# Performance work log

Measured on AMD Instinct MI355X. Metric: run time of the kernel, lower is better.

## Reference

```python
import jax, jax.numpy as jnp
import numpy as np

ROPE_THETA = 10000.0


def _rotate_half(x):
    # interleaved rotation: out[..., 2i] = -x[..., 2i+1], out[..., 2i+1] = x[..., 2i]
    x_even = x[..., ::2]
    x_odd = x[..., 1::2]
    return jnp.stack([-x_odd, x_even], axis=-1).reshape(x.shape)


def _rope_cos_sin(N, D, dtype):
    inv_freq = 1.0 / (ROPE_THETA ** (jnp.arange(0, D, 2, dtype=jnp.float32) / D))  # [D/2]
    angles = jnp.arange(N, dtype=jnp.float32)[:, None] * inv_freq[None, :]          # [N, D/2]
    angles = jnp.repeat(angles, 2, axis=-1)                                          # [N, D]
    cos = jnp.cos(angles).astype(dtype)[None, :, None, :]  # [1, N, 1, D]
    sin = jnp.sin(angles).astype(dtype)[None, :, None, :]
    return cos, sin


def setup_inputs() -> dict:
    key = jax.random.key(0)
    kq, kk, kv, km = jax.random.split(key, 4)
    B, N, H, D = 16, 1024, 8, 64
    xq = jax.random.normal(kq, (B, N, H, D), dtype=jnp.float32)
    xk = jax.random.normal(kk, (B, N, H, D), dtype=jnp.float32)
    xv = jax.random.normal(kv, (B, N, H, D), dtype=jnp.float32)
    vis_mask = jax.random.bernoulli(km, 0.8, (B, N))  # bool visibility mask per batch
    return {"xq": xq, "xk": xk, "xv": xv, "vis_mask": vis_mask}


def reference(xq, xk, xv, vis_mask):
    B, N, H, D = xq.shape
    sm_scale = 1.0 / np.sqrt(D).astype(np.float32)

    # RoPE (interleaved) on q and k
    cos, sin = _rope_cos_sin(N, D, xq.dtype)
    q = xq * cos + _rotate_half(xq) * sin
    k = xk * cos + _rotate_half(xk) * sin

    # masked full attention: scores [B, H, N, N]
    scores = jnp.einsum("bnhd,bmhd->bhnm", q, k) * sm_scale
    attn_mask = (vis_mask[:, None, :, None] & vis_mask[:, None, None, :])  # [B,1,N,N]
    scores = jnp.where(attn_mask, scores, -jnp.inf)
    p = jax.nn.softmax(scores, axis=-1)
    p = jnp.nan_to_num(p, nan=0.0)  # fully-masked rows -> zeros (matches fallback)
    out = jnp.einsum("bhnm,bmhd->bnhd", p, xv)
    return out
```

## Files before the change

kernel.cpp:

```cpp
#include <hip/hip_runtime.h>
#include <hip/hip_bf16.h>
#include <stdint.h>

#define Bb 16
#define Nn 1024
#define Hh 8
#define Dd 64

typedef unsigned short u16;
typedef float f32x4 __attribute__((ext_vector_type(4)));
typedef short short8 __attribute__((ext_vector_type(8)));

union U4S8 { uint4 u; short8 s; };
union BF2U { __hip_bfloat162 h; uint32_t u; };

__device__ __forceinline__ uint32_t f2bf(float f){
  union{float f;uint32_t i;} v; v.f=f;
  return (v.i + 0x7fffu + ((v.i>>16)&1u))>>16;
}

__device__ __forceinline__ f32x4 mfma16(short8 a, short8 b, f32x4 c){
  return __builtin_amdgcn_mfma_f32_16x16x32_bf16(a,b,c,0,0,0);
}

#define ROPE_K 0.41524101186092030f
#define QS 0.18033688011112042f
#define NEGBIG -1.0e30f

__global__ void rope_table_kernel(float2* __restrict__ tab){
  int id = blockIdx.x*256 + threadIdx.x;
  int n = id >> 5, i = id & 31;
  float inv = exp2f(-(float)i * ROPE_K);
  float a = (float)n * inv;
  float s, c; sincosf(a, &s, &c);
  tab[id] = make_float2(c, s);
}

__global__ __launch_bounds__(256) void prepass_kernel(
    const float* __restrict__ xk, const float* __restrict__ xv,
    const float2* __restrict__ tab,
    u16* __restrict__ Kr, u16* __restrict__ Vp)
{
  const int tid = threadIdx.x;
  const int bid = blockIdx.x;
  const int nt = bid & 15, h = (bid>>4)&7, b = bid>>7;
  const size_t bh = (size_t)b*Hh + h;

  {
    int r = tid>>2, c = (tid&3)<<4;
    int n = (nt<<6) + r;
    const float4* g = (const float4*)(xk + ((((size_t)b*Nn + n)*Hh + h)<<6) + c);
    float4 a0=g[0],a1=g[1],a2=g[2],a3=g[3];
    float xx[16] = {a0.x,a0.y,a0.z,a0.w, a1.x,a1.y,a1.z,a1.w,
                    a2.x,a2.y,a2.z,a2.w, a3.x,a3.y,a3.z,a3.w};
    uint32_t w[8];
    #pragma unroll
    for (int j=0;j<8;++j){
      int i = (c>>1)+j;
      float cs, sn;
      if (tab){ float2 t = tab[(n<<5)+i]; cs = t.x; sn = t.y; }
      else { float inv = exp2f(-(float)i * ROPE_K); sincosf((float)n*inv, &sn, &cs); }
      float x0 = xx[2*j], x1 = xx[2*j+1];
      float q0 = x0*cs - x1*sn;
      float q1 = x1*cs + x0*sn;
      w[j] = f2bf(q0) | (f2bf(q1)<<16);
    }
    u16* dst = Kr + (((bh<<10) + (size_t)n)<<6) + c;
    *(uint4*)dst     = make_uint4(w[0],w[1],w[2],w[3]);
    *(uint4*)(dst+8) = make_uint4(w[4],w[5],w[6],w[7]);
  }

  {
    int k = tid&63, ds = (tid>>6)<<4;
    int n = (nt<<6) + k;
    int slot = (k&1) | (((k>>4)&3)<<1) | (((k>>2)&3)<<3) | (((k>>1)&1)<<5);
    const float4* g = (const float4*)(xv + ((((size_t)b*Nn + n)*Hh + h)<<6) + ds);
    float4 a0=g[0],a1=g[1],a2=g[2],a3=g[3];
    float vv[16] = {a0.x,a0.y,a0.z,a0.w, a1.x,a1.y,a1.z,a1.w,
                    a2.x,a2.y,a2.z,a2.w, a3.x,a3.y,a3.z,a3.w};
    #pragma unroll
    for (int j=0;j<16;++j)
      Vp[ (bh<<16) + (nt<<12) + ((size_t)(ds+j)<<6) + slot ] = (u16)f2bf(vv[j]);
  }
}

__global__ __launch_bounds__(256,4) void attn4_kernel(
    const float* __restrict__ xq, const u16* __restrict__ Kr,
    const u16* __restrict__ Vp, const int* __restrict__ vis,
    const float2* __restrict__ tab, float* __restrict__ out)
{
  __shared__ u16 Ks[64][72];
  __shared__ u16 Vs[64][72];

  const int tid  = threadIdx.x;
  const int wave = tid >> 6;
  const int lane = tid & 63;
  const int l15  = lane & 15;
  const int quad = lane >> 4;

  const int bid = blockIdx.x;
  const int qt = bid & 7;
  const int h  = (bid >> 3) & 7;
  const int b  = bid >> 6;
  const size_t bh = (size_t)b*Hh + h;
  const int qbase = qt<<7;

  const int* visb = vis + b*Nn;

  short8 qa[2][2];
  #pragma unroll
  for (int mb=0; mb<2; ++mb){
    int n = qbase + (wave<<5) + (mb<<4) + l15;
    const float* src = xq + ((((size_t)b*Nn + n)*Hh + h)<<6);
    #pragma unroll
    for (int half=0; half<2; ++half){
      int d0 = (half<<5) + (quad<<3);
      const float4* g = (const float4*)(src + d0);
      float4 u0 = g[0], u1 = g[1];
      float xx[8] = {u0.x,u0.y,u0.z,u0.w, u1.x,u1.y,u1.z,u1.w};
      uint32_t w[4];
      #pragma unroll
      for (int j=0;j<4;++j){
        int i = (d0>>1) + j;
        float cs, sn;
        if (tab){ float2 t = tab[(n<<5)+i]; cs = t.x; sn = t.y; }
        else { float inv = exp2f(-(float)i * ROPE_K); sincosf((float)n*inv, &sn, &cs); }
        float x0 = xx[2*j], x1 = xx[2*j+1];
        float q0 = (x0*cs - x1*sn)*QS;
        float q1 = (x1*cs + x0*sn)*QS;
        w[j] = f2bf(q0) | (f2bf(q1)<<16);
      }
      U4S8 t; t.u = make_uint4(w[0],w[1],w[2],w[3]);
      qa[mb][half] = t.s;
    }
  }

  U4S8 ones_u; ones_u.u = make_uint4(0x3F803F80u,0x3F803F80u,0x3F803F80u,0x3F803F80u);
  const short8 ones = ones_u.s;

  f32x4 acc[2][4];
  f32x4 l_acc[2];
  #pragma unroll
  for (int mb=0;mb<2;++mb){
    l_acc[mb] = (f32x4){0.f,0.f,0.f,0.f};
    #pragma unroll
    for (int s=0;s<4;++s) acc[mb][s] = (f32x4){0.f,0.f,0.f,0.f};
  }

  const u16* Krb = Kr + (bh<<16);
  const u16* Vpb = Vp + (bh<<16);
  const int r = tid>>2, c16 = (tid&3)<<4;

  for (int kt=0; kt<16; ++kt){
    __syncthreads();
    {
      const u16* ksrc = Krb + (kt<<12) + (r<<6) + c16;
      uint4 k0 = *(const uint4*)ksrc, k1 = *(const uint4*)(ksrc+8);
      const u16* vsrc = Vpb + (kt<<12) + (r<<6) + c16;
      uint4 v0 = *(const uint4*)vsrc, v1 = *(const uint4*)(vsrc+8);
      *(uint4*)&Ks[r][c16]   = k0; *(uint4*)&Ks[r][c16+8] = k1;
      *(uint4*)&Vs[r][c16]   = v0; *(uint4*)&Vs[r][c16+8] = v1;
    }
    __syncthreads();

    uint32_t pk[4][2][2];
    #pragma unroll
    for (int kb=0;kb<4;++kb){
      short8 kf0 = *(const short8*)&Ks[(kb<<4)+l15][quad<<3];
      short8 kf1 = *(const short8*)&Ks[(kb<<4)+l15][(quad<<3)+32];
      int4 vi = *(const int4*)&visb[(kt<<6)+(kb<<4)+(quad<<2)];
      f32x4 bias;
      bias.x = vi.x ? 0.f : NEGBIG;
      bias.y = vi.y ? 0.f : NEGBIG;
      bias.z = vi.z ? 0.f : NEGBIG;
      bias.w = vi.w ? 0.f : NEGBIG;
      #pragma unroll
      for (int mb=0;mb<2;++mb){
        f32x4 t = mfma16(kf0, qa[mb][0], bias);
        t = mfma16(kf1, qa[mb][1], t);
        float p0 = __builtin_amdgcn_exp2f(t.x);
        float p1 = __builtin_amdgcn_exp2f(t.y);
        float p2 = __builtin_amdgcn_exp2f(t.z);
        float p3 = __builtin_amdgcn_exp2f(t.w);
        BF2U e0; e0.h = __float22bfloat162_rn(make_float2(p0,p1));
        BF2U e1; e1.h = __float22bfloat162_rn(make_float2(p2,p3));
        pk[kb][0][mb] = e0.u;
        pk[kb][1][mb] = e1.u;
      }
    }

    short8 pa[2][2];
    #pragma unroll
    for (int mb=0;mb<2;++mb){
      U4S8 a0; a0.u = make_uint4(pk[0][0][mb], pk[1][0][mb], pk[2][0][mb], pk[3][0][mb]);
      U4S8 a1; a1.u = make_uint4(pk[0][1][mb], pk[1][1][mb], pk[2][1][mb], pk[3][1][mb]);
      pa[mb][0] = a0.s; pa[mb][1] = a1.s;
    }

    #pragma unroll
    for (int mb=0;mb<2;++mb){
      l_acc[mb] = mfma16(pa[mb][0], ones, l_acc[mb]);
      l_acc[mb] = mfma16(pa[mb][1], ones, l_acc[mb]);
    }
    #pragma unroll
    for (int s=0;s<4;++s){
      short8 vb0 = *(const short8*)&Vs[(s<<4)+l15][quad<<3];
      short8 vb1 = *(const short8*)&Vs[(s<<4)+l15][(quad<<3)+32];
      #pragma unroll
      for (int mb=0;mb<2;++mb){
        acc[mb][s] = mfma16(pa[mb][0], vb0, acc[mb][s]);
        acc[mb][s] = mfma16(pa[mb][1], vb1, acc[mb][s]);
      }
    }
  }

  #pragma unroll
  for (int mb=0;mb<2;++mb){
    int4 qvi = *(const int4*)&visb[qbase + (wave<<5) + (mb<<4) + (quad<<2)];
    int qv[4] = {qvi.x, qvi.y, qvi.z, qvi.w};
    #pragma unroll
    for (int rr=0;rr<4;++rr){
      float lq = l_acc[mb][rr];
      float invl = (qv[rr] != 0 && lq > 0.f) ? 1.f/lq : 0.f;
      int qrow = qbase + (wave<<5) + (mb<<4) + (quad<<2) + rr;
      float* ob = out + ((((size_t)b*Nn + qrow)*Hh + h)<<6);
      #pragma unroll
      for (int s=0;s<4;++s)
        ob[(s<<4)+l15] = acc[mb][s][rr]*invl;
    }
  }
}

__device__ __forceinline__ void stage_rope_row_fb(const float* __restrict__ src,
                                                  u16 (*dst)[72],
                                                  int n_global, int sr, int d0)
{
  const float4* g = (const float4*)src;
  float4 a0 = g[0], a1 = g[1], a2 = g[2], a3 = g[3];
  float xx[16] = {a0.x,a0.y,a0.z,a0.w, a1.x,a1.y,a1.z,a1.w,
                  a2.x,a2.y,a2.z,a2.w, a3.x,a3.y,a3.z,a3.w};
  uint32_t w[8];
  #pragma unroll
  for (int j=0;j<8;++j){
    int i = (d0>>1)+j;
    float inv = exp2f(-(float)i * ROPE_K);
    float ang = (float)n_global * inv;
    float sn, cs; sincosf(ang, &sn, &cs);
    float x0 = xx[2*j], x1 = xx[2*j+1];
    float q0 = x0*cs - x1*sn;
    float q1 = x1*cs + x0*sn;
    w[j] = f2bf(q0) | (f2bf(q1)<<16);
  }
  *(uint4*)&dst[sr][d0]   = make_uint4(w[0],w[1],w[2],w[3]);
  *(uint4*)&dst[sr][d0+8] = make_uint4(w[4],w[5],w[6],w[7]);
}

__global__ __launch_bounds__(256,2) void attn_fallback(
    const float* __restrict__ xq, const float* __restrict__ xk,
    const float* __restrict__ xv, const int* __restrict__ vis,
    float* __restrict__ out)
{
  __shared__ u16 Qs[64][72];
  __shared__ u16 Ks[64][72];
  __shared__ u16 Vt[64][72];
  __shared__ u16 Ps[4][16][72];
  __shared__ float viss[64];

  const int tid  = threadIdx.x;
  const int wave = tid >> 6;
  const int lane = tid & 63;
  const int l15  = lane & 15;
  const int quad = lane >> 4;

  const int bid = blockIdx.x;
  const int qt = bid & 15;
  const int h  = (bid >> 4) & 7;
  const int b  = bid >> 7;

  const int sr = tid >> 2;
  const int d0 = (tid & 3) << 4;

  {
    int ng = (qt<<6) + sr;
    const float* src = xq + ((((size_t)b*Nn + ng)*Hh + h)<<6) + d0;
    stage_rope_row_fb(src, Qs, ng, sr, d0);
  }
  __syncthreads();

  short8 qa0 = *(const short8*)&Qs[(wave<<4)+l15][quad<<3];
  short8 qa1 = *(const short8*)&Qs[(wave<<4)+l15][(quad<<3)+32];

  f32x4 acc[4];
  #pragma unroll
  for (int s=0;s<4;++s) acc[s] = (f32x4){0.f,0.f,0.f,0.f};
  float m_r[4], l_r[4];
  #pragma unroll
  for (int rr=0;rr<4;++rr){ m_r[rr] = -1e30f; l_r[rr] = 0.f; }

  for (int kt=0; kt<16; ++kt){
    __syncthreads();
    {
      int ng = (kt<<6) + sr;
      const float* src = xk + ((((size_t)b*Nn + ng)*Hh + h)<<6) + d0;
      stage_rope_row_fb(src, Ks, ng, sr, d0);
    }
    {
      int ng = (kt<<6) + sr;
      const float4* g = (const float4*)(xv + ((((size_t)b*Nn + ng)*Hh + h)<<6) + d0);
      float4 a0 = g[0], a1 = g[1], a2 = g[2], a3 = g[3];
      float vv16[16] = {a0.x,a0.y,a0.z,a0.w, a1.x,a1.y,a1.z,a1.w,
                        a2.x,a2.y,a2.z,a2.w, a3.x,a3.y,a3.z,a3.w};
      #pragma unroll
      for (int j=0;j<16;++j) Vt[d0+j][sr] = (u16)f2bf(vv16[j]);
    }
    if (tid < 64) viss[tid] = (vis[b*Nn + (kt<<6) + tid] != 0) ? 1.f : 0.f;
    __syncthreads();

    f32x4 s4[4];
    #pragma unroll
    for (int n=0;n<4;++n){
      short8 kb0 = *(const short8*)&Ks[(n<<4)+l15][quad<<3];
      short8 kb1 = *(const short8*)&Ks[(n<<4)+l15][(quad<<3)+32];
      f32x4 t = (f32x4){0.f,0.f,0.f,0.f};
      t = mfma16(qa0, kb0, t);
      t = mfma16(qa1, kb1, t);
      s4[n] = t;
    }
    float vv[4];
    #pragma unroll
    for (int n=0;n<4;++n) vv[n] = viss[(n<<4)+l15];

    float p[4][4];
    #pragma unroll
    for (int rr=0; rr<4; ++rr){
      float sc[4];
      #pragma unroll
      for (int n=0;n<4;++n) sc[n] = (vv[n] > 0.f) ? s4[n][rr]*0.125f : -1e30f;
      float tm = fmaxf(fmaxf(sc[0],sc[1]), fmaxf(sc[2],sc[3]));
      tm = fmaxf(tm, __shfl_xor(tm,1));
      tm = fmaxf(tm, __shfl_xor(tm,2));
      tm = fmaxf(tm, __shfl_xor(tm,4));
      tm = fmaxf(tm, __shfl_xor(tm,8));
      float mnew  = fmaxf(m_r[rr], tm);
      float alpha = __expf(m_r[rr] - mnew);
      m_r[rr] = mnew;
      float psum = 0.f;
      #pragma unroll
      for (int n=0;n<4;++n){
        float pv = (vv[n] > 0.f) ? __expf(sc[n] - mnew) : 0.f;
        p[n][rr] = pv; psum += pv;
      }
      l_r[rr] = l_r[rr]*alpha + psum;
      #pragma unroll
      for (int s=0;s<4;++s) acc[s][rr] *= alpha;
    }

    #pragma unroll
    for (int n=0;n<4;++n)
      #pragma unroll
      for (int rr=0;rr<4;++rr)
        Ps[wave][(quad<<2)+rr][(n<<4)+l15] = (u16)f2bf(p[n][rr]);
    asm volatile("s_waitcnt lgkmcnt(0)" ::: "memory");
    short8 pa0 = *(const short8*)&Ps[wave][l15][quad<<3];
    short8 pa1 = *(const short8*)&Ps[wave][l15][(quad<<3)+32];

    #pragma unroll
    for (int s=0;s<4;++s){
      short8 vb0 = *(const short8*)&Vt[(s<<4)+l15][quad<<3];
      short8 vb1 = *(const short8*)&Vt[(s<<4)+l15][(quad<<3)+32];
      acc[s] = mfma16(pa0, vb0, acc[s]);
      acc[s] = mfma16(pa1, vb1, acc[s]);
    }
  }

  #pragma unroll
  for (int rr=0;rr<4;++rr){
    float t = l_r[rr];
    t += __shfl_xor(t,1); t += __shfl_xor(t,2);
    t += __shfl_xor(t,4); t += __shfl_xor(t,8);
    int row = (qt<<6) + (wave<<4) + (quad<<2) + rr;
    int qv  = vis[b*Nn + row];
    float invl = (qv != 0 && t > 0.f) ? 1.f/t : 0.f;
    size_t obase = (((size_t)b*Nn + row)*Hh + h) << 6;
    #pragma unroll
    for (int s=0;s<4;++s)
      out[obase + (s<<4) + l15] = acc[s][rr]*invl;
  }
}

extern "C" void kernel_launch(void* const* d_in, const int* in_sizes, int n_in,
                              void* d_out, int out_size, void* d_ws, size_t ws_size,
                              hipStream_t stream)
{
  const float* xq = (const float*)d_in[0];
  const float* xk = (const float*)d_in[1];
  const float* xv = (const float*)d_in[2];
  const int* vis  = (const int*)d_in[3];
  float* out = (float*)d_out;

  const size_t kv_elems = (size_t)Bb*Hh*Nn*Dd;
  const size_t kv_bytes = kv_elems*sizeof(u16);
  const size_t tab_bytes = (size_t)Nn*32*sizeof(float2);
  const size_t need_tab = tab_bytes + 2*kv_bytes;
  const size_t need_kv  = 2*kv_bytes;

  if (d_ws != nullptr && ws_size >= need_tab){
    float2* tab = (float2*)d_ws;
    u16* Kr = (u16*)((char*)d_ws + tab_bytes);
    u16* Vp = Kr + kv_elems;
    rope_table_kernel<<<dim3((Nn*32)/256), dim3(256), 0, stream>>>(tab);
    prepass_kernel<<<dim3(Bb*Hh*(Nn/64)), dim3(256), 0, stream>>>(xk, xv, tab, Kr, Vp);
    attn4_kernel<<<dim3(Bb*Hh*(Nn/128)), dim3(256), 0, stream>>>(xq, Kr, Vp, vis, tab, out);
  } else if (d_ws != nullptr && ws_size >= need_kv){
    u16* Kr = (u16*)d_ws;
    u16* Vp = Kr + kv_elems;
    prepass_kernel<<<dim3(Bb*Hh*(Nn/64)), dim3(256), 0, stream>>>(xk, xv, nullptr, Kr, Vp);
    attn4_kernel<<<dim3(Bb*Hh*(Nn/128)), dim3(256), 0, stream>>>(xq, Kr, Vp, vis, nullptr, out);
  } else {
    attn_fallback<<<dim3(Bb*Hh*(Nn/64)), dim3(256), 0, stream>>>(xq, xk, xv, vis, out);
  }
}
```

Before: 194.2 us.

## Pre-swizzle K/V into fragment order and double-buffer via direct global-to-LDS loads

```diff
diff --git a/kernel.cpp b/kernel.cpp
--- a/kernel.cpp
+++ b/kernel.cpp
@@ -21,6 +21,12 @@
 
 __device__ __forceinline__ f32x4 mfma16(short8 a, short8 b, f32x4 c){
   return __builtin_amdgcn_mfma_f32_16x16x32_bf16(a,b,c,0,0,0);
+}
+
+typedef __attribute__((address_space(3))) uint32_t lds_u32;
+typedef const __attribute__((address_space(1))) uint32_t glb_u32;
+__device__ __forceinline__ void gl_lds16(const u16* g, u16* l){
+  __builtin_amdgcn_global_load_lds((glb_u32*)g, (lds_u32*)l, 16, 0, 0);
 }
 
 #define ROPE_K 0.41524101186092030f
@@ -39,12 +45,13 @@
 __global__ __launch_bounds__(256) void prepass_kernel(
     const float* __restrict__ xk, const float* __restrict__ xv,
     const float2* __restrict__ tab,
-    u16* __restrict__ Kr, u16* __restrict__ Vp)
+    u16* __restrict__ Kf, u16* __restrict__ Vf)
 {
   const int tid = threadIdx.x;
   const int bid = blockIdx.x;
   const int nt = bid & 15, h = (bid>>4)&7, b = bid>>7;
   const size_t bh = (size_t)b*Hh + h;
+  const size_t tile = (bh<<4) + nt;
 
   {
     int r = tid>>2, c = (tid&3)<<4;
@@ -65,36 +72,43 @@
       float q1 = x1*cs + x0*sn;
       w[j] = f2bf(q0) | (f2bf(q1)<<16);
     }
-    u16* dst = Kr + (((bh<<10) + (size_t)n)<<6) + c;
-    *(uint4*)dst     = make_uint4(w[0],w[1],w[2],w[3]);
-    *(uint4*)(dst+8) = make_uint4(w[4],w[5],w[6],w[7]);
+    int kb = r>>4, l15 = r&15;
+    int half = c>>5, qd = (c>>3)&3;
+    u16* base = Kf + (tile<<12);
+    int dest0 = (kb<<10) + (half<<9) + (qd<<7) + (l15<<3);
+    *(uint4*)(base + dest0)       = make_uint4(w[0],w[1],w[2],w[3]);
+    *(uint4*)(base + dest0 + 128) = make_uint4(w[4],w[5],w[6],w[7]);
   }
 
   {
     int k = tid&63, ds = (tid>>6)<<4;
     int n = (nt<<6) + k;
     int slot = (k&1) | (((k>>4)&3)<<1) | (((k>>2)&3)<<3) | (((k>>1)&1)<<5);
+    int half = slot>>5, qd = (slot>>3)&3, j = slot&7;
     const float4* g = (const float4*)(xv + ((((size_t)b*Nn + n)*Hh + h)<<6) + ds);
     float4 a0=g[0],a1=g[1],a2=g[2],a3=g[3];
     float vv[16] = {a0.x,a0.y,a0.z,a0.w, a1.x,a1.y,a1.z,a1.w,
                     a2.x,a2.y,a2.z,a2.w, a3.x,a3.y,a3.z,a3.w};
-    #pragma unroll
-    for (int j=0;j<16;++j)
-      Vp[ (bh<<16) + (nt<<12) + ((size_t)(ds+j)<<6) + slot ] = (u16)f2bf(vv[j]);
-  }
-}
-
-__global__ __launch_bounds__(256,4) void attn4_kernel(
-    const float* __restrict__ xq, const u16* __restrict__ Kr,
-    const u16* __restrict__ Vp, const int* __restrict__ vis,
+    u16* base = Vf + (tile<<12);
+    #pragma unroll
+    for (int jj=0;jj<16;++jj){
+      int d = ds + jj;
+      int s = d>>4, l15v = d&15;
+      base[(s<<10) + (half<<9) + (qd<<7) + (l15v<<3) + j] = (u16)f2bf(vv[jj]);
+    }
+  }
+}
+
+__global__ __launch_bounds__(256,4) void attn5_kernel(
+    const float* __restrict__ xq, const u16* __restrict__ Kf,
+    const u16* __restrict__ Vf, const int* __restrict__ vis,
     const float2* __restrict__ tab, float* __restrict__ out)
 {
-  __shared__ u16 Ks[64][72];
-  __shared__ u16 Vs[64][72];
+  __shared__ u16 KV[2][2][4096];
 
   const int tid  = threadIdx.x;
+  const int lane = tid & 63;
   const int wave = tid >> 6;
-  const int lane = tid & 63;
   const int l15  = lane & 15;
   const int quad = lane >> 4;
 
@@ -106,6 +120,8 @@
   const int qbase = qt<<7;
 
   const int* visb = vis + b*Nn;
+  const u16* Kfb = Kf + (bh<<16);
+  const u16* Vfb = Vf + (bh<<16);
 
   short8 qa[2][2];
   #pragma unroll
@@ -147,27 +163,33 @@
     for (int s=0;s<4;++s) acc[mb][s] = (f32x4){0.f,0.f,0.f,0.f};
   }
 
-  const u16* Krb = Kr + (bh<<16);
-  const u16* Vpb = Vp + (bh<<16);
-  const int r = tid>>2, c16 = (tid&3)<<4;
+  const int t8 = tid<<3;
+
+  {
+    const u16* kg = Kfb;  const u16* vg = Vfb;
+    gl_lds16(kg + t8,        &KV[0][0][t8]);
+    gl_lds16(kg + 2048 + t8, &KV[0][0][2048 + t8]);
+    gl_lds16(vg + t8,        &KV[0][1][t8]);
+    gl_lds16(vg + 2048 + t8, &KV[0][1][2048 + t8]);
+  }
+  __syncthreads();
 
   for (int kt=0; kt<16; ++kt){
-    __syncthreads();
-    {
-      const u16* ksrc = Krb + (kt<<12) + (r<<6) + c16;
-      uint4 k0 = *(const uint4*)ksrc, k1 = *(const uint4*)(ksrc+8);
-      const u16* vsrc = Vpb + (kt<<12) + (r<<6) + c16;
-      uint4 v0 = *(const uint4*)vsrc, v1 = *(const uint4*)(vsrc+8);
-      *(uint4*)&Ks[r][c16]   = k0; *(uint4*)&Ks[r][c16+8] = k1;
-      *(uint4*)&Vs[r][c16]   = v0; *(uint4*)&Vs[r][c16+8] = v1;
-    }
-    __syncthreads();
+    const int cur = kt & 1;
+    if (kt < 15){
+      const u16* kg = Kfb + ((kt+1)<<12);
+      const u16* vg = Vfb + ((kt+1)<<12);
+      gl_lds16(kg + t8,        &KV[cur^1][0][t8]);
+      gl_lds16(kg + 2048 + t8, &KV[cur^1][0][2048 + t8]);
+      gl_lds16(vg + t8,        &KV[cur^1][1][t8]);
+      gl_lds16(vg + 2048 + t8, &KV[cur^1][1][2048 + t8]);
+    }
 
     uint32_t pk[4][2][2];
     #pragma unroll
     for (int kb=0;kb<4;++kb){
-      short8 kf0 = *(const short8*)&Ks[(kb<<4)+l15][quad<<3];
-      short8 kf1 = *(const short8*)&Ks[(kb<<4)+l15][(quad<<3)+32];
+      short8 kf0 = *(const short8*)&KV[cur][0][(kb<<10) + (lane<<3)];
+      short8 kf1 = *(const short8*)&KV[cur][0][(kb<<10) + 512 + (lane<<3)];
       int4 vi = *(const int4*)&visb[(kt<<6)+(kb<<4)+(quad<<2)];
       f32x4 bias;
       bias.x = vi.x ? 0.f : NEGBIG;
@@ -204,14 +226,16 @@
     }
     #pragma unroll
     for (int s=0;s<4;++s){
-      short8 vb0 = *(const short8*)&Vs[(s<<4)+l15][quad<<3];
-      short8 vb1 = *(const short8*)&Vs[(s<<4)+l15][(quad<<3)+32];
+      short8 vb0 = *(const short8*)&KV[cur][1][(s<<10) + (lane<<3)];
+      short8 vb1 = *(const short8*)&KV[cur][1][(s<<10) + 512 + (lane<<3)];
       #pragma unroll
       for (int mb=0;mb<2;++mb){
         acc[mb][s] = mfma16(pa[mb][0], vb0, acc[mb][s]);
         acc[mb][s] = mfma16(pa[mb][1], vb1, acc[mb][s]);
       }
     }
+
+    __syncthreads();
   }
 
   #pragma unroll
@@ -406,16 +430,16 @@
 
   if (d_ws != nullptr && ws_size >= need_tab){
     float2* tab = (float2*)d_ws;
-    u16* Kr = (u16*)((char*)d_ws + tab_bytes);
-    u16* Vp = Kr + kv_elems;
+    u16* Kf = (u16*)((char*)d_ws + tab_bytes);
+    u16* Vf = Kf + kv_elems;
     rope_table_kernel<<<dim3((Nn*32)/256), dim3(256), 0, stream>>>(tab);
-    prepass_kernel<<<dim3(Bb*Hh*(Nn/64)), dim3(256), 0, stream>>>(xk, xv, tab, Kr, Vp);
-    attn4_kernel<<<dim3(Bb*Hh*(Nn/128)), dim3(256), 0, stream>>>(xq, Kr, Vp, vis, tab, out);
+    prepass_kernel<<<dim3(Bb*Hh*(Nn/64)), dim3(256), 0, stream>>>(xk, xv, tab, Kf, Vf);
+    attn5_kernel<<<dim3(Bb*Hh*(Nn/128)), dim3(256), 0, stream>>>(xq, Kf, Vf, vis, tab, out);
   } else if (d_ws != nullptr && ws_size >= need_kv){
-    u16* Kr = (u16*)d_ws;
-    u16* Vp = Kr + kv_elems;
-    prepass_kernel<<<dim3(Bb*Hh*(Nn/64)), dim3(256), 0, stream>>>(xk, xv, nullptr, Kr, Vp);
-    attn4_kernel<<<dim3(Bb*Hh*(Nn/128)), dim3(256), 0, stream>>>(xq, Kr, Vp, vis, nullptr, out);
+    u16* Kf = (u16*)d_ws;
+    u16* Vf = Kf + kv_elems;
+    prepass_kernel<<<dim3(Bb*Hh*(Nn/64)), dim3(256), 0, stream>>>(xk, xv, nullptr, Kf, Vf);
+    attn5_kernel<<<dim3(Bb*Hh*(Nn/128)), dim3(256), 0, stream>>>(xq, Kf, Vf, vis, nullptr, out);
   } else {
     attn_fallback<<<dim3(Bb*Hh*(Nn/64)), dim3(256), 0, stream>>>(xq, xk, xv, vis, out);
   }
```

Result: slower. 207.5 us (+6.9%).
